# Kernel optimization log

Hardware: AMD Instinct MI355X
Metric: run time of the kernel (lower is better)

Reference implementation:

```python
import jax, jax.numpy as jnp
import numpy as np
from jax import lax

B, N, C, H, W, HEADS = 8, 4096, 512, 64, 64, 16
HD = C // HEADS
BN_EPS = 1e-5


def _dwconv3x3(x, w, b):
    # x: (B,C,H,W), w: (C,1,3,3) depthwise conv, padding=1
    y = lax.conv_general_dilated(x, w, (1, 1), 'SAME',
                                 dimension_numbers=('NCHW', 'OIHW', 'NCHW'),
                                 feature_group_count=x.shape[1])
    return y + b[None, :, None, None]


def _spatial_op(x, dw_w, dw_b, bn_g, bn_b, pw_w):
    # SpatialOperation: dwconv -> BN(eval, mean=0,var=1) -> ReLU -> 1x1 conv to 1 ch -> sigmoid gate
    y = _dwconv3x3(x, dw_w, dw_b)
    y = y * (bn_g * (1.0 / np.sqrt(1.0 + BN_EPS)))[None, :, None, None] + bn_b[None, :, None, None]
    y = jax.nn.relu(y)
    s = jax.nn.sigmoid(jnp.einsum('bchw,c->bhw', y, pw_w))[:, None]  # (B,1,H,W)
    return x * s


def _channel_op(x, w):
    # ChannelOperation: global avg pool -> 1x1 conv (c->c) -> sigmoid gate
    pool = x.mean(axis=(2, 3))                      # (B,C)
    s = jax.nn.sigmoid(jnp.einsum('bc,oc->bo', pool, w))
    return x * s[:, :, None, None]


def _rope(x, cos, sin):
    # x: (B,H,W,C); pairs of consecutive channels form complex numbers
    xr = x[..., 0::2]
    xi = x[..., 1::2]
    re = cos * xr - sin * xi
    im = sin * xr + cos * xi
    return jnp.stack([re, im], axis=-1).reshape(x.shape)


def setup_inputs():
    key = jax.random.key(0)
    ks = jax.random.split(key, 16)
    def p(k, shape, scale=0.02):
        return jax.random.normal(k, shape, dtype=jnp.float32) * scale
    inp = {
        'x': jax.random.normal(ks[0], (B, N, C), dtype=jnp.float32),
        'qk_w': p(ks[1], (2 * C, C)),
        'qk_b': p(ks[2], (2 * C,)),
        'qsp_dw_w': p(ks[3], (C, 1, 3, 3), 0.1),
        'qsp_dw_b': p(ks[4], (C,)),
        'qsp_bn_g': jnp.ones((C,), jnp.float32),
        'qsp_bn_b': jnp.zeros((C,), jnp.float32),
        'qsp_pw_w': p(ks[5], (C,), 0.05),
        'qch_w': p(ks[6], (C, C)),
        'ksp_dw_w': p(ks[7], (C, 1, 3, 3), 0.1),
        'ksp_dw_b': p(ks[8], (C,)),
        'ksp_bn_g': jnp.ones((C,), jnp.float32),
        'ksp_bn_b': jnp.zeros((C,), jnp.float32),
        'ksp_pw_w': p(ks[9], (C,), 0.05),
        'kch_w': p(ks[10], (C, C)),
        'lepe_w': p(ks[11], (C, 1, 3, 3), 0.1),
        'lepe_b': p(ks[12], (C,)),
    }
    # RoPE buffers, exactly as torch __init__: k_max = C // (2*2)
    kmax = C // 4
    theta = 1.0 / (10000.0 ** (np.arange(kmax) / kmax))
    hi, wi = np.meshgrid(np.arange(H), np.arange(W), indexing='ij')
    angles = np.concatenate([hi[..., None] * theta, wi[..., None] * theta], axis=-1)  # (H,W,C//2)
    inp['rope_cos'] = jnp.asarray(np.cos(angles), jnp.float32)
    inp['rope_sin'] = jnp.asarray(np.sin(angles), jnp.float32)
    return inp


def reference(x, qk_w, qk_b, qsp_dw_w, qsp_dw_b, qsp_bn_g, qsp_bn_b, qsp_pw_w, qch_w,
              ksp_dw_w, ksp_dw_b, ksp_bn_g, ksp_bn_b, ksp_pw_w, kch_w,
              lepe_w, lepe_b, rope_cos, rope_sin):
    b, n, c = x.shape
    qk = x @ qk_w.T + qk_b                          # (b,n,2c)
    q_proj, k_proj = qk[..., :c], qk[..., c:]
    q_nchw = jnp.transpose(q_proj, (0, 2, 1)).reshape(b, c, H, W)
    k_nchw = jnp.transpose(k_proj, (0, 2, 1)).reshape(b, c, H, W)
    q_nchw = _channel_op(_spatial_op(q_nchw, qsp_dw_w, qsp_dw_b, qsp_bn_g, qsp_bn_b, qsp_pw_w), qch_w)
    k_nchw = _channel_op(_spatial_op(k_nchw, ksp_dw_w, ksp_dw_b, ksp_bn_g, ksp_bn_b, ksp_pw_w), kch_w)
    q = jnp.transpose(q_nchw.reshape(b, c, n), (0, 2, 1))
    k = jnp.transpose(k_nchw.reshape(b, c, n), (0, 2, 1))
    q = jax.nn.elu(q) + 1.0
    k = jax.nn.elu(k) + 1.0
    q_rope = _rope(q.reshape(b, H, W, c), rope_cos, rope_sin).reshape(b, n, HEADS, HD).transpose(0, 2, 1, 3)
    k_rope = _rope(k.reshape(b, H, W, c), rope_cos, rope_sin).reshape(b, n, HEADS, HD).transpose(0, 2, 1, 3)
    v = x.reshape(b, n, HEADS, HD).transpose(0, 2, 1, 3)   # (b,h,n,d)
    k_mean = k_rope.mean(axis=2, keepdims=True)             # (b,h,1,d)
    z = 1.0 / (jnp.einsum('bhnd,bhmd->bhnm', q_rope, k_mean) + 1e-6)  # (b,h,n,1)
    kv = jnp.einsum('bhnd,bhne->bhde', k_rope, v) / n       # (b,h,d,d)
    out = jnp.einsum('bhnd,bhde->bhne', q_rope, kv) * z     # (b,h,n,d)
    out = out.transpose(0, 2, 1, 3).reshape(b, n, c)
    v_nchw = v.transpose(0, 2, 1, 3).reshape(b, H, W, c).transpose(0, 3, 1, 2)
    lepe = _dwconv3x3(v_nchw, lepe_w, lepe_b).transpose(0, 2, 3, 1).reshape(b, n, c)
    return out + lepe
```

## Files before the change

kernel.cpp:

```cpp
#include <hip/hip_runtime.h>
#include <cmath>

namespace {

constexpr int CH    = 512;
constexpr int NPIX  = 4096;

typedef _Float16 half8 __attribute__((ext_vector_type(8)));
typedef _Float16 half4 __attribute__((ext_vector_type(4)));
typedef float    f32x4 __attribute__((ext_vector_type(4)));

__device__ __forceinline__ float sigmoidf_(float v) { return 1.0f / (1.0f + expf(-v)); }

__global__ __launch_bounds__(256) void k_split(
    const float4* __restrict__ in, half4* __restrict__ hi,
    half4* __restrict__ lo, int n4)
{
    int i = blockIdx.x * 256 + threadIdx.x;
    if (i >= n4) return;
    float4 v = in[i];
    half4 h, l;
    h[0] = (_Float16)v.x; l[0] = (_Float16)((v.x - (float)h[0]) * 1024.0f);
    h[1] = (_Float16)v.y; l[1] = (_Float16)((v.y - (float)h[1]) * 1024.0f);
    h[2] = (_Float16)v.z; l[2] = (_Float16)((v.z - (float)h[2]) * 1024.0f);
    h[3] = (_Float16)v.w; l[3] = (_Float16)((v.w - (float)h[3]) * 1024.0f);
    hi[i] = h; lo[i] = l;
}

__global__ __launch_bounds__(256, 2) void k_gemm_mfma(
    const _Float16* __restrict__ Ahi, const _Float16* __restrict__ Alo,
    const _Float16* __restrict__ Bhi, const _Float16* __restrict__ Blo,
    const float* __restrict__ bias, float* __restrict__ out)
{
    __shared__ _Float16 lds[4 * 128 * 32];
    const int t    = threadIdx.x;
    const int wave = t >> 6;
    const int lane = t & 63;
    const int bm   = blockIdx.x;
    const int bn   = blockIdx.y;

    const _Float16* src;
    switch (wave) {
        case 0: src = Ahi + (size_t)bm * 128 * 512; break;
        case 1: src = Alo + (size_t)bm * 128 * 512; break;
        case 2: src = Bhi + (size_t)bn * 128 * 512; break;
        default: src = Blo + (size_t)bn * 128 * 512; break;
    }
    const _Float16* srcLane = src + (size_t)(lane >> 2) * 512 + (lane & 3) * 8;
    _Float16* ldsW = lds + wave * 4096;

    const int wm = wave >> 1, wn = wave & 1;
    const int mrow = lane & 15;
    const int kq   = (lane >> 4) * 8;
    const _Float16* aH = lds         + (wm * 64 + mrow) * 32 + kq;
    const _Float16* aL = lds + 4096  + (wm * 64 + mrow) * 32 + kq;
    const _Float16* bH = lds + 8192  + (wn * 64 + mrow) * 32 + kq;
    const _Float16* bL = lds + 12288 + (wn * 64 + mrow) * 32 + kq;

    f32x4 acc0[4][4], acc1[4][4];
    #pragma unroll
    for (int i = 0; i < 4; i++)
        #pragma unroll
        for (int j = 0; j < 4; j++) { acc0[i][j] = (f32x4)0.0f; acc1[i][j] = (f32x4)0.0f; }

    for (int k0 = 0; k0 < 16; k0++) {
        const _Float16* g = srcLane + k0 * 32;
        #pragma unroll
        for (int r = 0; r < 8; r++) {
            __builtin_amdgcn_global_load_lds(
                (const __attribute__((address_space(1))) void*)(g + (size_t)r * 16 * 512),
                (__attribute__((address_space(3))) void*)(ldsW + r * 512),
                16, 0, 0);
        }
        __syncthreads();

        half8 ah[4], al[4], bh[4], bl[4];
        #pragma unroll
        for (int i = 0; i < 4; i++) {
            ah[i] = *(const half8*)(aH + i * 16 * 32);
            al[i] = *(const half8*)(aL + i * 16 * 32);
            bh[i] = *(const half8*)(bH + i * 16 * 32);
            bl[i] = *(const half8*)(bL + i * 16 * 32);
        }
        #pragma unroll
        for (int i = 0; i < 4; i++)
            #pragma unroll
            for (int j = 0; j < 4; j++) {
                acc0[i][j] = __builtin_amdgcn_mfma_f32_16x16x32_f16(ah[i], bh[j], acc0[i][j], 0, 0, 0);
                acc1[i][j] = __builtin_amdgcn_mfma_f32_16x16x32_f16(ah[i], bl[j], acc1[i][j], 0, 0, 0);
                acc1[i][j] = __builtin_amdgcn_mfma_f32_16x16x32_f16(al[i], bh[j], acc1[i][j], 0, 0, 0);
            }
        __syncthreads();
    }

    const int ccol = lane & 15;
    const int crow = (lane >> 4) * 4;
    #pragma unroll
    for (int j = 0; j < 4; j++) {
        int col = bn * 128 + wn * 64 + j * 16 + ccol;
        float bv = bias[col];
        #pragma unroll
        for (int i = 0; i < 4; i++) {
            size_t row0 = (size_t)bm * 128 + wm * 64 + i * 16 + crow;
            #pragma unroll
            for (int r = 0; r < 4; r++) {
                float v = acc0[i][j][r] + acc1[i][j][r] * (1.0f / 1024.0f) + bv;
                out[(row0 + r) * 1024 + col] = v;
            }
        }
    }
}

__global__ __launch_bounds__(512) void k_spatial(
    const float* __restrict__ qk,
    const float* __restrict__ dw_w_q, const float* __restrict__ dw_b_q,
    const float* __restrict__ bn_g_q, const float* __restrict__ bn_b_q,
    const float* __restrict__ pw_q,
    const float* __restrict__ dw_w_k, const float* __restrict__ dw_b_k,
    const float* __restrict__ bn_g_k, const float* __restrict__ bn_b_k,
    const float* __restrict__ pw_k,
    float* __restrict__ s_sp_q, float* __restrict__ s_sp_k,
    float* __restrict__ pool_q, float* __restrict__ pool_k)
{
    const int which = blockIdx.y;
    const int bx = blockIdx.x;
    const int b  = bx >> 8;
    const int h  = (bx >> 2) & 63;
    const int w0 = (bx & 3) * 16;
    const int c  = threadIdx.x;
    const float* dw_w = which ? dw_w_k : dw_w_q;
    const float* dw_b = which ? dw_b_k : dw_b_q;
    const float* bn_g = which ? bn_g_k : bn_g_q;
    const float* bn_b = which ? bn_b_k : bn_b_q;
    const float* pw   = which ? pw_k   : pw_q;
    float*       s_sp = which ? s_sp_k : s_sp_q;
    float*       pool = which ? pool_k : pool_q;

    float w9[9];
    #pragma unroll
    for (int j = 0; j < 9; j++) w9[j] = dw_w[c * 9 + j];
    const float bconv = dw_b[c];
    const float bns   = bn_g[c] * (1.0f / sqrtf(1.00001f));
    const float bnb   = bn_b[c];
    const float pwc   = pw[c];

    __shared__ float wavepart[16][8];
    __shared__ float s_row[16];
    const int lane = c & 63, wid = c >> 6;
    const float* inb  = qk + (size_t)b * NPIX * 1024 + (which ? 512 : 0);
    const float* row0 = inb + (size_t)(h * 64) * 1024 + c;
    const float* rowm = row0 - (ptrdiff_t)64 * 1024;
    const float* rowp = row0 + (ptrdiff_t)64 * 1024;
    const bool hm_ok = (h > 0), hp_ok = (h < 63);

    float x0m, x00, x0p, x1m, x10, x1p, x2m, x20, x2p;
    float cent[16];

    auto LD3 = [&](int wg, float& vm, float& v0, float& vp) {
        bool wok = (wg >= 0) && (wg < 64);
        ptrdiff_t o = (ptrdiff_t)wg * 1024;
        vm = (wok && hm_ok) ? rowm[o] : 0.0f;
        v0 =  wok           ? row0[o] : 0.0f;
        vp = (wok && hp_ok) ? rowp[o] : 0.0f;
    };

    LD3(w0 - 1, x0m, x1m, x2m);
    LD3(w0,     x00, x10, x20);

    #pragma unroll
    for (int i = 0; i < 16; i++) {
        LD3(w0 + i + 1, x0p, x1p, x2p);
        float y = bconv;
        y = fmaf(x0m, w9[0], y); y = fmaf(x00, w9[1], y); y = fmaf(x0p, w9[2], y);
        y = fmaf(x1m, w9[3], y); y = fmaf(x10, w9[4], y); y = fmaf(x1p, w9[5], y);
        y = fmaf(x2m, w9[6], y); y = fmaf(x20, w9[7], y); y = fmaf(x2p, w9[8], y);
        y = fmaxf(fmaf(y, bns, bnb), 0.0f);
        cent[i] = x10;
        float contrib = y * pwc;
        #pragma unroll
        for (int o = 32; o > 0; o >>= 1) contrib += __shfl_down(contrib, o, 64);
        if (lane == 0) wavepart[i][wid] = contrib;
        x0m = x00; x00 = x0p;
        x1m = x10; x10 = x1p;
        x2m = x20; x20 = x2p;
    }
    __syncthreads();
    if (c < 16) {
        float s = 0.0f;
        #pragma unroll
        for (int j = 0; j < 8; j++) s += wavepart[c][j];
        s = sigmoidf_(s);
        s_row[c] = s;
        s_sp[(size_t)b * NPIX + h * 64 + w0 + c] = s;
    }
    __syncthreads();
    float pacc = 0.0f;
    #pragma unroll
    for (int i = 0; i < 16; i++) pacc = fmaf(cent[i], s_row[i], pacc);
    atomicAdd(&pool[(size_t)b * CH + c], pacc);
}

__global__ __launch_bounds__(256) void k_chsig(
    const float* __restrict__ pool_q, const float* __restrict__ pool_k,
    const float* __restrict__ qch_w,  const float* __restrict__ kch_w,
    float* __restrict__ sch_q, float* __restrict__ sch_k)
{
    int id    = blockIdx.x;
    int which = id >> 10;
    int rem   = id & 1023;
    int b     = rem >> 7;
    int og    = rem & 127;
    int wid   = threadIdx.x >> 6, lane = threadIdx.x & 63;
    int o     = og * 4 + wid;
    const float* pool = which ? pool_k : pool_q;
    const float* Wt   = which ? kch_w  : qch_w;
    float s = 0.0f;
    for (int cc = lane; cc < CH; cc += 64) s = fmaf(pool[b * CH + cc], Wt[o * CH + cc], s);
    #pragma unroll
    for (int off = 32; off > 0; off >>= 1) s += __shfl_down(s, off, 64);
    if (lane == 0)
        (which ? sch_k : sch_q)[b * CH + o] = sigmoidf_(s * (1.0f / 4096.0f));
}

__global__ __launch_bounds__(512) void k_rope(
    float* __restrict__ qk,
    const float* __restrict__ s_sp_q, const float* __restrict__ s_sp_k,
    const float* __restrict__ sch_q,  const float* __restrict__ sch_k,
    const float* __restrict__ cosT,   const float* __restrict__ sinT,
    float* __restrict__ kmean)
{
    const int which = blockIdx.y;
    const int c = threadIdx.x;
    const int pix0 = blockIdx.x * 8;
    const int b  = pix0 >> 12;
    const int n0 = pix0 & 4095;
    float* buf = qk + (which ? 512 : 0);
    const float* s_sp = which ? s_sp_k : s_sp_q;
    const float  sch  = (which ? sch_k : sch_q)[b * CH + c];
    const int kidx = c >> 1;
    const int odd  = c & 1;
    float kacc = 0.0f;
    #pragma unroll
    for (int p = 0; p < 8; p++) {
        int n = n0 + p;
        float ssp = s_sp[(size_t)b * NPIX + n];
        size_t idx = ((size_t)b * NPIX + n) * 1024 + c;
        float v = buf[idx] * ssp * sch;
        float e = v > 0.0f ? v + 1.0f : expf(v);
        float part = __shfl_xor(e, 1, 64);
        float cs = cosT[(size_t)n * 256 + kidx];
        float sn = sinT[(size_t)n * 256 + kidx];
        float r = odd ? fmaf(sn, part, cs * e) : fmaf(cs, e, -(sn * part));
        buf[idx] = r;
        if (which) kacc += r;
    }
    if (which) atomicAdd(&kmean[(size_t)b * CH + c], kacc);
}

__global__ __launch_bounds__(256) void k_kv(
    const float* __restrict__ qk, const float* __restrict__ x,
    float* __restrict__ kv)
{
    const int bh = blockIdx.x;
    const int b  = bh >> 4, hh = bh & 15;
    const int n0 = blockIdx.y * 512;
    __shared__ float kt[32][33];
    __shared__ float vt[32][33];
    const int t  = threadIdx.x;
    const int e  = t & 31, d0 = (t >> 5) * 4;
    const int nn  = t >> 3;
    const int cc4 = (t & 7) * 4;
    float acc[4] = {0.f, 0.f, 0.f, 0.f};
    for (int s = 0; s < 512; s += 32) {
        size_t rowbase = ((size_t)(b * NPIX + n0 + s + nn));
        float4 kvv = *(const float4*)(qk + rowbase * 1024 + 512 + hh * 32 + cc4);
        kt[nn][cc4] = kvv.x; kt[nn][cc4+1] = kvv.y; kt[nn][cc4+2] = kvv.z; kt[nn][cc4+3] = kvv.w;
        float4 vv  = *(const float4*)(x + rowbase * 512 + hh * 32 + cc4);
        vt[nn][cc4] = vv.x; vt[nn][cc4+1] = vv.y; vt[nn][cc4+2] = vv.z; vt[nn][cc4+3] = vv.w;
        __syncthreads();
        #pragma unroll
        for (int q = 0; q < 32; q++) {
            float vq = vt[q][e];
            acc[0] = fmaf(kt[q][d0    ], vq, acc[0]);
            acc[1] = fmaf(kt[q][d0 + 1], vq, acc[1]);
            acc[2] = fmaf(kt[q][d0 + 2], vq, acc[2]);
            acc[3] = fmaf(kt[q][d0 + 3], vq, acc[3]);
        }
        __syncthreads();
    }
    #pragma unroll
    for (int i = 0; i < 4; i++)
        atomicAdd(&kv[((size_t)bh * 32 + d0 + i) * 32 + e], acc[i]);
}

__global__ __launch_bounds__(512) void k_final(
    const float* __restrict__ qk, const float* __restrict__ x,
    const float* __restrict__ kvbuf, const float* __restrict__ kmean,
    const float* __restrict__ lepe_w, const float* __restrict__ lepe_b,
    float* __restrict__ out)
{
    const int bx = blockIdx.x;
    const int b  = bx >> 7;
    const int h  = (bx >> 1) & 63;
    const int w0 = (bx & 1) * 32;
    const int c  = threadIdx.x;
    const int e  = c & 31;
    const int head = c >> 5;

    float kvreg[32];
    #pragma unroll
    for (int d = 0; d < 32; d++)
        kvreg[d] = kvbuf[((size_t)b * 16 + head) * 1024 + d * 32 + e] * (1.0f / 4096.0f);
    const float km = kmean[(size_t)b * CH + c] * (1.0f / 4096.0f);
    float w9[9];
    #pragma unroll
    for (int j = 0; j < 9; j++) w9[j] = lepe_w[c * 9 + j];
    const float lb = lepe_b[c];

    const float* xr0 = x + ((size_t)b * NPIX + h * 64) * 512 + c;
    const float* xrm = xr0 - (ptrdiff_t)64 * 512;
    const float* xrp = xr0 + (ptrdiff_t)64 * 512;
    const bool hm_ok = (h > 0), hp_ok = (h < 63);
    const float* qkb = qk + ((size_t)b * NPIX + h * 64) * 1024 + c;
    float* outb = out + ((size_t)b * NPIX + h * 64) * 512 + c;

    float x0m, x00, x0p, x1m, x10, x1p, x2m, x20, x2p;
    auto LD3 = [&](int wg, float& vm, float& v0, float& vp) {
        bool wok = (wg >= 0) && (wg < 64);
        ptrdiff_t o = (ptrdiff_t)wg * 512;
        vm = (wok && hm_ok) ? xrm[o] : 0.0f;
        v0 =  wok           ? xr0[o] : 0.0f;
        vp = (wok && hp_ok) ? xrp[o] : 0.0f;
    };
    LD3(w0 - 1, x0m, x1m, x2m);
    LD3(w0,     x00, x10, x20);

    for (int i = 0; i < 32; i++) {
        const int wg = w0 + i;
        float x0p_, x1p_, x2p_;
        LD3(wg + 1, x0p_, x1p_, x2p_);
        x0p = x0p_; x1p = x1p_; x2p = x2p_;

        float qv = qkb[(size_t)wg * 1024];
        float den = qv * km;
        #pragma unroll
        for (int off = 16; off > 0; off >>= 1) den += __shfl_xor(den, off, 32);
        float z = 1.0f / (den + 1e-6f);
        float num = 0.0f;
        #pragma unroll
        for (int d = 0; d < 32; d++) num = fmaf(__shfl(qv, d, 32), kvreg[d], num);

        float lp = lb;
        lp = fmaf(x0m, w9[0], lp); lp = fmaf(x00, w9[1], lp); lp = fmaf(x0p, w9[2], lp);
        lp = fmaf(x1m, w9[3], lp); lp = fmaf(x10, w9[4], lp); lp = fmaf(x1p, w9[5], lp);
        lp = fmaf(x2m, w9[6], lp); lp = fmaf(x20, w9[7], lp); lp = fmaf(x2p, w9[8], lp);

        outb[(size_t)wg * 512] = fmaf(num, z, lp);

        x0m = x00; x00 = x0p;
        x1m = x10; x10 = x1p;
        x2m = x20; x20 = x2p;
    }
}

}

extern "C" void kernel_launch(void* const* d_in, const int* in_sizes, int n_in,
                              void* d_out, int out_size, void* d_ws, size_t ws_size,
                              hipStream_t stream)
{
    (void)in_sizes; (void)n_in; (void)out_size; (void)ws_size;
    const float* x        = (const float*)d_in[0];
    const float* qk_w     = (const float*)d_in[1];
    const float* qk_b     = (const float*)d_in[2];
    const float* qsp_dw_w = (const float*)d_in[3];
    const float* qsp_dw_b = (const float*)d_in[4];
    const float* qsp_bn_g = (const float*)d_in[5];
    const float* qsp_bn_b = (const float*)d_in[6];
    const float* qsp_pw_w = (const float*)d_in[7];
    const float* qch_w    = (const float*)d_in[8];
    const float* ksp_dw_w = (const float*)d_in[9];
    const float* ksp_dw_b = (const float*)d_in[10];
    const float* ksp_bn_g = (const float*)d_in[11];
    const float* ksp_bn_b = (const float*)d_in[12];
    const float* ksp_pw_w = (const float*)d_in[13];
    const float* kch_w    = (const float*)d_in[14];
    const float* lepe_w   = (const float*)d_in[15];
    const float* lepe_b   = (const float*)d_in[16];
    const float* rope_cos = (const float*)d_in[17];
    const float* rope_sin = (const float*)d_in[18];

    float* ws     = (float*)d_ws;
    float* qk     = ws;
    float* s_sp_q = qk + 33554432;
    float* s_sp_k = s_sp_q + 32768;
    float* sch_q  = s_sp_k + 32768;
    float* sch_k  = sch_q + 4096;
    float* pool_q = sch_k + 4096;
    float* pool_k = pool_q + 4096;
    float* kmean  = pool_k + 4096;
    float* kv     = kmean + 4096;
    _Float16* x_hi = (_Float16*)(kv + 131072);
    _Float16* x_lo = x_hi + 16777216;
    _Float16* w_hi = x_lo + 16777216;
    _Float16* w_lo = w_hi + 524288;

    hipMemsetAsync(pool_q, 0, (size_t)(3 * 4096 + 131072) * sizeof(float), stream);

    k_split<<<16384, 256, 0, stream>>>((const float4*)x, (half4*)x_hi, (half4*)x_lo, 4194304);
    k_split<<<512, 256, 0, stream>>>((const float4*)qk_w, (half4*)w_hi, (half4*)w_lo, 131072);
    k_gemm_mfma<<<dim3(256, 8), 256, 0, stream>>>(x_hi, x_lo, w_hi, w_lo, qk_b, qk);

    k_spatial<<<dim3(2048, 2), 512, 0, stream>>>(qk,
        qsp_dw_w, qsp_dw_b, qsp_bn_g, qsp_bn_b, qsp_pw_w,
        ksp_dw_w, ksp_dw_b, ksp_bn_g, ksp_bn_b, ksp_pw_w,
        s_sp_q, s_sp_k, pool_q, pool_k);
    k_chsig<<<2048, 256, 0, stream>>>(pool_q, pool_k, qch_w, kch_w, sch_q, sch_k);
    k_rope<<<dim3(4096, 2), 512, 0, stream>>>(qk, s_sp_q, s_sp_k, sch_q, sch_k,
                                              rope_cos, rope_sin, kmean);
    k_kv<<<dim3(128, 8), 256, 0, stream>>>(qk, x, kv);
    k_final<<<1024, 512, 0, stream>>>(qk, x, kv, kmean, lepe_w, lepe_b, (float*)d_out);
}
```

Measured before the change: 543.7 us.

## Fuse gating, ELU and RoPE into kv and final kernels, drop k_rope

Removes the standalone k_rope kernel, which read and rewrote the whole 8x4096x1024 qk buffer. The k-side gating, ELU+1, RoPE and k-mean accumulation now run while k_kv loads tiles. The q-side transform runs inline in k_final before the attention dot product. This saves a full read-modify-write pass over qk and one launch, at the cost of extra ALU work and cos/sin loads inside the consuming kernels.

```diff
diff --git a/kernel.cpp b/kernel.cpp
--- a/kernel.cpp
+++ b/kernel.cpp
@@ -222,44 +222,11 @@
         (which ? sch_k : sch_q)[b * CH + o] = sigmoidf_(s * (1.0f / 4096.0f));
 }
 
-__global__ __launch_bounds__(512) void k_rope(
-    float* __restrict__ qk,
-    const float* __restrict__ s_sp_q, const float* __restrict__ s_sp_k,
-    const float* __restrict__ sch_q,  const float* __restrict__ sch_k,
-    const float* __restrict__ cosT,   const float* __restrict__ sinT,
-    float* __restrict__ kmean)
-{
-    const int which = blockIdx.y;
-    const int c = threadIdx.x;
-    const int pix0 = blockIdx.x * 8;
-    const int b  = pix0 >> 12;
-    const int n0 = pix0 & 4095;
-    float* buf = qk + (which ? 512 : 0);
-    const float* s_sp = which ? s_sp_k : s_sp_q;
-    const float  sch  = (which ? sch_k : sch_q)[b * CH + c];
-    const int kidx = c >> 1;
-    const int odd  = c & 1;
-    float kacc = 0.0f;
-    #pragma unroll
-    for (int p = 0; p < 8; p++) {
-        int n = n0 + p;
-        float ssp = s_sp[(size_t)b * NPIX + n];
-        size_t idx = ((size_t)b * NPIX + n) * 1024 + c;
-        float v = buf[idx] * ssp * sch;
-        float e = v > 0.0f ? v + 1.0f : expf(v);
-        float part = __shfl_xor(e, 1, 64);
-        float cs = cosT[(size_t)n * 256 + kidx];
-        float sn = sinT[(size_t)n * 256 + kidx];
-        float r = odd ? fmaf(sn, part, cs * e) : fmaf(cs, e, -(sn * part));
-        buf[idx] = r;
-        if (which) kacc += r;
-    }
-    if (which) atomicAdd(&kmean[(size_t)b * CH + c], kacc);
-}
-
 __global__ __launch_bounds__(256) void k_kv(
     const float* __restrict__ qk, const float* __restrict__ x,
-    float* __restrict__ kv)
+    const float* __restrict__ s_sp_k, const float* __restrict__ sch_k,
+    const float* __restrict__ cosT,   const float* __restrict__ sinT,
+    float* __restrict__ kv, float* __restrict__ kmean)
 {
     const int bh = blockIdx.x;
     const int b  = bh >> 4, hh = bh & 15;
@@ -270,12 +237,40 @@
     const int e  = t & 31, d0 = (t >> 5) * 4;
     const int nn  = t >> 3;
     const int cc4 = (t & 7) * 4;
+    const int cg  = hh * 32 + cc4;
+    const int kidx = cg >> 1;
+
+    const float sch0 = sch_k[b * CH + cg + 0];
+    const float sch1 = sch_k[b * CH + cg + 1];
+    const float sch2 = sch_k[b * CH + cg + 2];
+    const float sch3 = sch_k[b * CH + cg + 3];
+
+    float km0 = 0.f, km1 = 0.f, km2 = 0.f, km3 = 0.f;
     float acc[4] = {0.f, 0.f, 0.f, 0.f};
     for (int s = 0; s < 512; s += 32) {
-        size_t rowbase = ((size_t)(b * NPIX + n0 + s + nn));
-        float4 kvv = *(const float4*)(qk + rowbase * 1024 + 512 + hh * 32 + cc4);
-        kt[nn][cc4] = kvv.x; kt[nn][cc4+1] = kvv.y; kt[nn][cc4+2] = kvv.z; kt[nn][cc4+3] = kvv.w;
-        float4 vv  = *(const float4*)(x + rowbase * 512 + hh * 32 + cc4);
+        const int n = n0 + s + nn;
+        size_t rowbase = (size_t)(b * NPIX + n);
+        float4 kvv = *(const float4*)(qk + rowbase * 1024 + 512 + cg);
+        const float ssp = s_sp_k[(size_t)b * NPIX + n];
+        float g0 = kvv.x * ssp * sch0;
+        float g1 = kvv.y * ssp * sch1;
+        float g2 = kvv.z * ssp * sch2;
+        float g3 = kvv.w * ssp * sch3;
+        float e0 = g0 > 0.0f ? g0 + 1.0f : expf(g0);
+        float e1 = g1 > 0.0f ? g1 + 1.0f : expf(g1);
+        float e2 = g2 > 0.0f ? g2 + 1.0f : expf(g2);
+        float e3 = g3 > 0.0f ? g3 + 1.0f : expf(g3);
+        const float cs0 = cosT[(size_t)n * 256 + kidx];
+        const float sn0 = sinT[(size_t)n * 256 + kidx];
+        const float cs1 = cosT[(size_t)n * 256 + kidx + 1];
+        const float sn1 = sinT[(size_t)n * 256 + kidx + 1];
+        float r0 = fmaf(cs0, e0, -(sn0 * e1));
+        float r1 = fmaf(sn0, e0,   cs0 * e1);
+        float r2 = fmaf(cs1, e2, -(sn1 * e3));
+        float r3 = fmaf(sn1, e2,   cs1 * e3);
+        kt[nn][cc4] = r0; kt[nn][cc4+1] = r1; kt[nn][cc4+2] = r2; kt[nn][cc4+3] = r3;
+        km0 += r0; km1 += r1; km2 += r2; km3 += r3;
+        float4 vv  = *(const float4*)(x + rowbase * 512 + cg);
         vt[nn][cc4] = vv.x; vt[nn][cc4+1] = vv.y; vt[nn][cc4+2] = vv.z; vt[nn][cc4+3] = vv.w;
         __syncthreads();
         #pragma unroll
@@ -291,11 +286,17 @@
     #pragma unroll
     for (int i = 0; i < 4; i++)
         atomicAdd(&kv[((size_t)bh * 32 + d0 + i) * 32 + e], acc[i]);
+    atomicAdd(&kmean[(size_t)b * CH + cg + 0], km0);
+    atomicAdd(&kmean[(size_t)b * CH + cg + 1], km1);
+    atomicAdd(&kmean[(size_t)b * CH + cg + 2], km2);
+    atomicAdd(&kmean[(size_t)b * CH + cg + 3], km3);
 }
 
 __global__ __launch_bounds__(512) void k_final(
     const float* __restrict__ qk, const float* __restrict__ x,
     const float* __restrict__ kvbuf, const float* __restrict__ kmean,
+    const float* __restrict__ s_sp_q, const float* __restrict__ sch_q,
+    const float* __restrict__ cosT,   const float* __restrict__ sinT,
     const float* __restrict__ lepe_w, const float* __restrict__ lepe_b,
     float* __restrict__ out)
 {
@@ -306,12 +307,15 @@
     const int c  = threadIdx.x;
     const int e  = c & 31;
     const int head = c >> 5;
+    const int kidx = c >> 1;
+    const int odd  = c & 1;
 
     float kvreg[32];
     #pragma unroll
     for (int d = 0; d < 32; d++)
         kvreg[d] = kvbuf[((size_t)b * 16 + head) * 1024 + d * 32 + e] * (1.0f / 4096.0f);
     const float km = kmean[(size_t)b * CH + c] * (1.0f / 4096.0f);
+    const float schc = sch_q[(size_t)b * CH + c];
     float w9[9];
     #pragma unroll
     for (int j = 0; j < 9; j++) w9[j] = lepe_w[c * 9 + j];
@@ -322,6 +326,9 @@
     const float* xrp = xr0 + (ptrdiff_t)64 * 512;
     const bool hm_ok = (h > 0), hp_ok = (h < 63);
     const float* qkb = qk + ((size_t)b * NPIX + h * 64) * 1024 + c;
+    const float* ssb = s_sp_q + (size_t)b * NPIX + h * 64;
+    const float* csb = cosT + (size_t)(h * 64) * 256 + kidx;
+    const float* snb = sinT + (size_t)(h * 64) * 256 + kidx;
     float* outb = out + ((size_t)b * NPIX + h * 64) * 512 + c;
 
     float x0m, x00, x0p, x1m, x10, x1p, x2m, x20, x2p;
@@ -341,7 +348,15 @@
         LD3(wg + 1, x0p_, x1p_, x2p_);
         x0p = x0p_; x1p = x1p_; x2p = x2p_;
 
-        float qv = qkb[(size_t)wg * 1024];
+        float qraw = qkb[(size_t)wg * 1024];
+        float ssp  = ssb[wg];
+        float g    = qraw * ssp * schc;
+        float eV   = g > 0.0f ? g + 1.0f : expf(g);
+        float part = __shfl_xor(eV, 1, 64);
+        float cs   = csb[(size_t)wg * 256];
+        float sn   = snb[(size_t)wg * 256];
+        float qv   = odd ? fmaf(sn, part, cs * eV) : fmaf(cs, eV, -(sn * part));
+
         float den = qv * km;
         #pragma unroll
         for (int off = 16; off > 0; off >>= 1) den += __shfl_xor(den, off, 32);
@@ -353,9 +368,9 @@
         float lp = lb;
         lp = fmaf(x0m, w9[0], lp); lp = fmaf(x00, w9[1], lp); lp = fmaf(x0p, w9[2], lp);
         lp = fmaf(x1m, w9[3], lp); lp = fmaf(x10, w9[4], lp); lp = fmaf(x1p, w9[5], lp);
-        lp = fmaf(x2m, w9[6], lp); lp = fmaf(x20, w9[7], lp); lp = fmaf(x2p, w9[8], lp);
-
-        outb[(size_t)wg * 512] = fmaf(num, z, lp);
+        lp = fmaf(x2m, w9[6], lp); lp = fmaf(x20, w9[7], lp);
+
+        outb[(size_t)wg * 512] = fmaf(num, z, fmaf(x2p, w9[8], lp));
 
         x0m = x00; x00 = x0p;
         x1m = x10; x10 = x1p;
@@ -416,8 +431,8 @@
         ksp_dw_w, ksp_dw_b, ksp_bn_g, ksp_bn_b, ksp_pw_w,
         s_sp_q, s_sp_k, pool_q, pool_k);
     k_chsig<<<2048, 256, 0, stream>>>(pool_q, pool_k, qch_w, kch_w, sch_q, sch_k);
-    k_rope<<<dim3(4096, 2), 512, 0, stream>>>(qk, s_sp_q, s_sp_k, sch_q, sch_k,
-                                              rope_cos, rope_sin, kmean);
-    k_kv<<<dim3(128, 8), 256, 0, stream>>>(qk, x, kv);
-    k_final<<<1024, 512, 0, stream>>>(qk, x, kv, kmean, lepe_w, lepe_b, (float*)d_out);
-}
+    k_kv<<<dim3(128, 8), 256, 0, stream>>>(qk, x, s_sp_k, sch_k, rope_cos, rope_sin,
+                                           kv, kmean);
+    k_final<<<1024, 512, 0, stream>>>(qk, x, kv, kmean, s_sp_q, sch_q,
+                                      rope_cos, rope_sin, lepe_w, lepe_b, (float*)d_out);
+}
```

Result: faster. 521.9 us (-4.0%).
